# Kernel optimization log

Measured on AMD Instinct MI355X. Metric: run time of the kernel, lower is better.

## Reference

```python
import jax, jax.numpy as jnp
import numpy as np

D = 1024      # feature_dim
H = 16        # heads
HD = D // H   # head_dim
B, N = 8, 1024
LN_EPS = 1e-5


def setup_inputs() -> dict:
    key = jax.random.key(0)
    ks = jax.random.split(key, 12)
    s = 0.02
    return {
        "x": jax.random.normal(ks[0], (B, N, D), jnp.float32),
        "Wq": jax.random.normal(ks[1], (D, D), jnp.float32) * s,
        "bq": jnp.zeros((D,), jnp.float32),
        "Wk": jax.random.normal(ks[2], (D, D), jnp.float32) * s,
        "bk": jnp.zeros((D,), jnp.float32),
        "Wv": jax.random.normal(ks[3], (D, D), jnp.float32) * s,
        "bv": jnp.zeros((D,), jnp.float32),
        "pair_bias": jnp.zeros((D, D), jnp.float32),  # init zeros as in torch
        "Wo": jax.random.normal(ks[4], (D, D), jnp.float32) * s,
        "bo": jnp.zeros((D,), jnp.float32),
        "gamma": jnp.ones((D,), jnp.float32),
        "beta": jnp.zeros((D,), jnp.float32),
    }


def reference(x, Wq, bq, Wk, bk, Wv, bv, pair_bias, Wo, bo, gamma, beta):
    b, n, d = x.shape
    residual = x
    # projections -> [b, h, n, hd]
    def split_heads(t):
        return t.reshape(b, n, H, HD).transpose(0, 2, 1, 3)
    q = split_heads(x @ Wq + bq)
    k = split_heads(x @ Wk + bk)
    v = split_heads(x @ Wv + bv)
    # scores + shared pairwise bias (same bias for every batch/head)
    scores = jnp.einsum('bhqd,bhkd->bhqk', q, k) / jnp.sqrt(jnp.float32(HD))
    scores = scores + pair_bias[:n, :n][None, None, :, :]
    attn = jax.nn.softmax(scores, axis=-1)
    # dropout in eval mode == identity
    out = jnp.einsum('bhqk,bhkd->bhqd', attn, v)
    out = out.transpose(0, 2, 1, 3).reshape(b, n, d)
    out = out @ Wo + bo
    out = residual + out
    # LayerNorm
    mu = jnp.mean(out, axis=-1, keepdims=True)
    var = jnp.var(out, axis=-1, keepdims=True)
    out = (out - mu) * jax.lax.rsqrt(var + LN_EPS) * gamma + beta
    return out, attn
```

## Files before the change

### kernel.cpp

```cpp
#include <hip/hip_runtime.h>
#include <hip/hip_bf16.h>
#include <stdint.h>
#include <stddef.h>

#define DI __device__ __forceinline__

typedef unsigned short u16;
typedef float f32x4 __attribute__((ext_vector_type(4)));
typedef short bf16x8 __attribute__((ext_vector_type(8)));
typedef u16 u16x4 __attribute__((ext_vector_type(4)));

constexpr int Mm = 8192;
constexpr int Dd = 1024;
constexpr float LOG2E = 1.44269504088896f;

DI u16 bf(float f) {
  __hip_bfloat16 h = __float2bfloat16(f);
  return *reinterpret_cast<u16*>(&h);
}

DI float b2f(short s) {
  union { float f; unsigned u; } v;
  v.u = ((unsigned)(unsigned short)s) << 16;
  return v.f;
}

DI f32x4 mfma16(bf16x8 a, bf16x8 b, f32x4 c) {
  return __builtin_amdgcn_mfma_f32_16x16x32_bf16(a, b, c, 0, 0, 0);
}

DI void gload16(const u16* g, u16* l) {
  __builtin_amdgcn_global_load_lds(
      (const __attribute__((address_space(1))) void*)(g),
      (__attribute__((address_space(3))) void*)(l), 16, 0, 0);
}

__global__ __launch_bounds__(256) void k_prep(const float* __restrict__ x,
                                              u16* __restrict__ xb,
                                              const float* __restrict__ pb,
                                              u16* __restrict__ pbb,
                                              const float* __restrict__ W0,
                                              const float* __restrict__ W1,
                                              const float* __restrict__ W2,
                                              const float* __restrict__ W3,
                                              u16* __restrict__ T0,
                                              u16* __restrict__ T1,
                                              u16* __restrict__ T2,
                                              u16* __restrict__ T3) {
  __shared__ float t[32][33];
  const int bid = blockIdx.x;
  const int tid = threadIdx.x;
  if (bid < 8192) {
    size_t i = (size_t)bid * 256 + tid;
    float4 v = *(const float4*)(x + i * 4);
    u16x4 r;
    r.x = bf(v.x); r.y = bf(v.y); r.z = bf(v.z); r.w = bf(v.w);
    *(u16x4*)(xb + i * 4) = r;
  } else if (bid < 9216) {
    size_t i = (size_t)(bid - 8192) * 256 + tid;
    float4 v = *(const float4*)(pb + i * 4);
    u16x4 r;
    r.x = bf(v.x * LOG2E); r.y = bf(v.y * LOG2E);
    r.z = bf(v.z * LOG2E); r.w = bf(v.w * LOG2E);
    *(u16x4*)(pbb + i * 4) = r;
  } else {
    const int tt = bid - 9216;
    const int z = tt >> 10;
    const int rem = tt & 1023;
    const float* W;
    u16* T;
    switch (z) {
      case 0: W = W0; T = T0; break;
      case 1: W = W1; T = T1; break;
      case 2: W = W2; T = T2; break;
      default: W = W3; T = T3; break;
    }
    const int bx = (rem & 31) * 32;
    const int by = (rem >> 5) * 32;
    const int tx = tid & 31, ty = tid >> 5;
#pragma unroll
    for (int i = 0; i < 4; ++i)
      t[ty + i * 8][tx] = W[(size_t)(bx + ty + i * 8) * 1024 + by + tx];
    __syncthreads();
#pragma unroll
    for (int i = 0; i < 4; ++i)
      T[(size_t)(by + ty + i * 8) * 1024 + bx + tx] = bf(t[tx][ty + i * 8]);
  }
}

__global__ __launch_bounds__(256) void k_gemm_qkv(const u16* __restrict__ A,
                                                  const u16* __restrict__ wqT,
                                                  const u16* __restrict__ wkT,
                                                  const u16* __restrict__ wvT,
                                                  const float* __restrict__ bq,
                                                  const float* __restrict__ bk,
                                                  const float* __restrict__ bv,
                                                  u16* __restrict__ qo,
                                                  u16* __restrict__ ko,
                                                  u16* __restrict__ vo) {
  __shared__ __align__(16) u16 smem[2 * 128 * 64];
  u16* As = smem;
  u16* Bs = smem + 128 * 64;
  const int bid = blockIdx.x;
  const int wgid = (bid & 7) * 192 + (bid >> 3);
  const int mode = wgid >> 9;
  const int rem = wgid & 511;
  const int brow = (rem >> 3) * 128;
  const int bcol = (rem & 7) * 128;
  const u16* WT = mode == 0 ? wqT : (mode == 1 ? wkT : wvT);
  const float* bias = mode == 0 ? bq : (mode == 1 ? bk : bv);
  const int tid = threadIdx.x;
  const int lane = tid & 63;
  const int wave = tid >> 6;
  const int wr = (wave >> 1) * 64;
  const int wc = (wave & 1) * 64;
  const int l15 = lane & 15, l4 = lane >> 4;

  f32x4 acc[4][4] = {};
  const int crow0 = tid >> 3;
  const int kpos = (tid & 7) * 8;

  for (int t = 0; t < 16; ++t) {
    const int k0 = t * 64;
#pragma unroll
    for (int r = 0; r < 4; ++r) {
      int crow = r * 32 + crow0;
      u16* ldsbase_a = As + ((r * 256 + wave * 64) << 3);
      u16* ldsbase_b = Bs + ((r * 256 + wave * 64) << 3);
      gload16(A + (size_t)(brow + crow) * 1024 + k0 + kpos, ldsbase_a);
      gload16(WT + (size_t)(bcol + crow) * 1024 + k0 + kpos, ldsbase_b);
    }
    __syncthreads();
#pragma unroll
    for (int kk = 0; kk < 2; ++kk) {
      bf16x8 af[4], bg[4];
      const int kb = kk * 32 + l4 * 8;
#pragma unroll
      for (int mt = 0; mt < 4; ++mt)
        af[mt] = *(const bf16x8*)(As + (wr + mt * 16 + l15) * 64 + kb);
#pragma unroll
      for (int nt = 0; nt < 4; ++nt)
        bg[nt] = *(const bf16x8*)(Bs + (wc + nt * 16 + l15) * 64 + kb);
#pragma unroll
      for (int mt = 0; mt < 4; ++mt)
#pragma unroll
        for (int nt = 0; nt < 4; ++nt)
          acc[mt][nt] = mfma16(af[mt], bg[nt], acc[mt][nt]);
    }
    __syncthreads();
  }

  if (mode == 2) {
#pragma unroll
    for (int nt = 0; nt < 4; ++nt) {
      int dl = wc + nt * 16 + l15;
      float bvv = bias[bcol + dl];
#pragma unroll
      for (int mt = 0; mt < 4; ++mt) {
        int s4 = wr + mt * 16 + l4 * 4;
        u16x4 pk;
        pk.x = bf(acc[mt][nt][0] + bvv);
        pk.y = bf(acc[mt][nt][1] + bvv);
        pk.z = bf(acc[mt][nt][2] + bvv);
        pk.w = bf(acc[mt][nt][3] + bvv);
        *(u16x4*)(smem + dl * 128 + (s4 ^ ((dl & 7) << 3))) = pk;
      }
    }
    __syncthreads();
    const int bb = brow >> 10;
    const int seq0 = brow & 1023;
    const int chunk = tid & 15;
#pragma unroll
    for (int p = 0; p < 8; ++p) {
      int dl = p * 16 + (tid >> 4);
      bf16x8 v = *(const bf16x8*)(smem + dl * 128 + ((chunk * 8) ^ ((dl & 7) << 3)));
      *(bf16x8*)(vo + ((size_t)bb * 1024 + bcol + dl) * 1024 + seq0 + chunk * 8) = v;
    }
    return;
  }

  u16* outp = mode == 0 ? qo : ko;
  const float scale = mode == 0 ? (0.125f * LOG2E) : 1.0f;
#pragma unroll
  for (int nt = 0; nt < 4; ++nt) {
    int gc = bcol + wc + nt * 16 + l15;
    float bvv = bias[gc];
#pragma unroll
    for (int mt = 0; mt < 4; ++mt) {
#pragma unroll
      for (int i = 0; i < 4; ++i) {
        int gm = brow + wr + mt * 16 + l4 * 4 + i;
        outp[(size_t)gm * 1024 + gc] = bf((acc[mt][nt][i] + bvv) * scale);
      }
    }
  }
}

__global__ __launch_bounds__(256) void k_gemm_o(const u16* __restrict__ A,
                                                const u16* __restrict__ WT,
                                                const float* __restrict__ bias,
                                                const float* __restrict__ resid,
                                                float* __restrict__ outp) {
  __shared__ __align__(16) u16 smem[2 * 128 * 64];
  u16* As = smem;
  u16* Bs = smem + 128 * 64;
  const int bid = blockIdx.x;
  const int wgid = (bid & 7) * 64 + (bid >> 3);
  const int brow = (wgid >> 3) * 128;
  const int bcol = (wgid & 7) * 128;
  const int tid = threadIdx.x;
  const int lane = tid & 63;
  const int wave = tid >> 6;
  const int wr = (wave >> 1) * 64;
  const int wc = (wave & 1) * 64;
  const int l15 = lane & 15, l4 = lane >> 4;

  f32x4 acc[4][4] = {};
  const int crow0 = tid >> 3;
  const int kpos = (tid & 7) * 8;

  for (int t = 0; t < 16; ++t) {
    const int k0 = t * 64;
#pragma unroll
    for (int r = 0; r < 4; ++r) {
      int crow = r * 32 + crow0;
      u16* ldsbase_a = As + ((r * 256 + wave * 64) << 3);
      u16* ldsbase_b = Bs + ((r * 256 + wave * 64) << 3);
      gload16(A + (size_t)(brow + crow) * 1024 + k0 + kpos, ldsbase_a);
      gload16(WT + (size_t)(bcol + crow) * 1024 + k0 + kpos, ldsbase_b);
    }
    __syncthreads();
#pragma unroll
    for (int kk = 0; kk < 2; ++kk) {
      bf16x8 af[4], bg[4];
      const int kb = kk * 32 + l4 * 8;
#pragma unroll
      for (int mt = 0; mt < 4; ++mt)
        af[mt] = *(const bf16x8*)(As + (wr + mt * 16 + l15) * 64 + kb);
#pragma unroll
      for (int nt = 0; nt < 4; ++nt)
        bg[nt] = *(const bf16x8*)(Bs + (wc + nt * 16 + l15) * 64 + kb);
#pragma unroll
      for (int mt = 0; mt < 4; ++mt)
#pragma unroll
        for (int nt = 0; nt < 4; ++nt)
          acc[mt][nt] = mfma16(af[mt], bg[nt], acc[mt][nt]);
    }
    __syncthreads();
  }

#pragma unroll
  for (int nt = 0; nt < 4; ++nt) {
    int gc = bcol + wc + nt * 16 + l15;
    float bvv = bias[gc];
#pragma unroll
    for (int mt = 0; mt < 4; ++mt) {
#pragma unroll
      for (int i = 0; i < 4; ++i) {
        int gm = brow + wr + mt * 16 + l4 * 4 + i;
        outp[(size_t)gm * 1024 + gc] =
            acc[mt][nt][i] + bvv + resid[(size_t)gm * 1024 + gc];
      }
    }
  }
}

__global__ __launch_bounds__(256, 3) void k_attn(const u16* __restrict__ q,
                                                 const u16* __restrict__ kk_,
                                                 const u16* __restrict__ vt,
                                                 const u16* __restrict__ pbb,
                                                 float* __restrict__ attn_out,
                                                 u16* __restrict__ aout) {
  __shared__ __align__(16) u16 sc[16 * 1024];
  __shared__ __align__(16) u16 kst[8192];
  __shared__ float invbuf[16];
  const int tid = threadIdx.x;
  const int lane = tid & 63;
  const int wave = tid >> 6;
  const int bid = blockIdx.x;
  const int swz = (bid & 7) * 1024 + (bid >> 3);
  const int bh = swz >> 6;
  const int q0 = (swz & 63) * 16;
  const int b = bh >> 4, h = bh & 15;
  const int l15 = lane & 15, l4 = lane >> 4;
  const int srow8 = (lane >> 3) & 7;
  const int sgsw = (lane & 7) ^ srow8;

  bf16x8 qf0, qf1;
  {
    const u16* qp = q + ((size_t)(b * 1024 + q0 + l15)) * 1024 + h * 64 + l4 * 8;
    qf0 = *(const bf16x8*)qp;
    qf1 = *(const bf16x8*)(qp + 32);
  }

  {
    u16* const kw = kst + wave * 2048;
    const int kvb = wave * 256;
    const u16* kbase = kk_ + (size_t)(b * 1024 + kvb) * 1024 + h * 64 + sgsw * 8;
    gload16(kbase + (size_t)srow8 * 1024, kw);
    gload16(kbase + (size_t)(8 + srow8) * 1024, kw + 512);
    for (int c = 0; c < 16; ++c) {
      if (c < 15) {
        const u16* nsrc = kbase + (size_t)((c + 1) * 16 + srow8) * 1024;
        u16* ndst = kw + ((c + 1) & 1) * 1024;
        gload16(nsrc, ndst);
        gload16(nsrc + 8 * 1024, ndst + 512);
        asm volatile("s_waitcnt vmcnt(2)" ::: "memory");
      } else {
        asm volatile("s_waitcnt vmcnt(0)" ::: "memory");
      }
      __builtin_amdgcn_sched_barrier(0);
      const u16* kb = kw + (c & 1) * 1024;
      const int r = l15;
      bf16x8 k0 = *(const bf16x8*)(kb + r * 64 + ((l4 ^ (r & 7)) << 3));
      bf16x8 k1 = *(const bf16x8*)(kb + r * 64 + (((4 + l4) ^ (r & 7)) << 3));
      f32x4 cc = {};
      cc = mfma16(k0, qf0, cc);
      cc = mfma16(k1, qf1, cc);
      const int c4 = kvb + c * 16 + l4 * 4;
      u16x4 pk;
      pk.x = bf(cc[0]); pk.y = bf(cc[1]); pk.z = bf(cc[2]); pk.w = bf(cc[3]);
      *(u16x4*)(sc + l15 * 1024 + (c4 ^ ((l15 & 7) << 3))) = pk;
    }
  }
  __syncthreads();

  const u16* vbase2 = vt + (size_t)(b * 1024 + h * 64 + wave * 32 + srow8) * 1024 + sgsw * 8;
  u16* const kw3 = kst + wave * 4096;
  if (wave < 2) {
#pragma unroll
    for (int i = 0; i < 4; ++i)
      gload16(vbase2 + (size_t)(i * 8) * 1024, kw3 + i * 512);
  }

  const int r2 = tid >> 4;
  const int l2 = tid & 15;
  {
    const int rx = (r2 & 7) << 3;
    u16* rowp = sc + r2 * 1024;
    const u16* pbrow = pbb + (size_t)(q0 + r2) * 1024 + l2 * 8;
    bf16x8 R[8];
#pragma unroll
    for (int g = 0; g < 8; ++g) {
      bf16x8 v = *(const bf16x8*)(rowp + ((g * 128 + l2 * 8) ^ rx));
      bf16x8 pv = *(const bf16x8*)(pbrow + g * 128);
      bf16x8 s;
#pragma unroll
      for (int j = 0; j < 8; ++j) s[j] = (short)bf(b2f(v[j]) + b2f(pv[j]));
      R[g] = s;
    }
    float mx = -3e38f;
#pragma unroll
    for (int g = 0; g < 8; ++g)
#pragma unroll
      for (int j = 0; j < 8; ++j) mx = fmaxf(mx, b2f(R[g][j]));
#pragma unroll
    for (int o = 1; o < 16; o <<= 1) mx = fmaxf(mx, __shfl_xor(mx, o));
    float sum = 0.f;
#pragma unroll
    for (int g = 0; g < 8; ++g) {
      bf16x8 e;
#pragma unroll
      for (int j = 0; j < 8; ++j) {
        float t = exp2f(b2f(R[g][j]) - mx);
        sum += t;
        e[j] = (short)bf(t);
      }
      *(bf16x8*)(rowp + ((g * 128 + l2 * 8) ^ rx)) = e;
    }
#pragma unroll
    for (int o = 1; o < 16; o <<= 1) sum += __shfl_xor(sum, o);
    if (l2 == 0) invbuf[r2] = 1.f / sum;
  }
  __syncthreads();

  if (wave < 2) {
    f32x4 oacc[2] = {};
    for (int c = 0; c < 16; ++c) {
      if (c < 15) {
        const u16* nsrc = vbase2 + (c + 1) * 64;
        u16* ndst = kw3 + ((c + 1) & 1) * 2048;
#pragma unroll
        for (int i = 0; i < 4; ++i)
          gload16(nsrc + (size_t)(i * 8) * 1024, ndst + i * 512);
        asm volatile("s_waitcnt vmcnt(4)" ::: "memory");
      } else {
        asm volatile("s_waitcnt vmcnt(0)" ::: "memory");
      }
      __builtin_amdgcn_sched_barrier(0);
      const u16* vb = kw3 + (c & 1) * 2048;
#pragma unroll
      for (int ks = 0; ks < 2; ++ks) {
        const int gg = ks * 4 + l4;
        const int e = c * 64 + ks * 32 + l4 * 8;
        bf16x8 pf = *(const bf16x8*)(sc + l15 * 1024 + (e ^ ((l15 & 7) << 3)));
#pragma unroll
        for (int dg = 0; dg < 2; ++dg) {
          const int vr = dg * 16 + l15;
          bf16x8 vf = *(const bf16x8*)(vb + vr * 64 + ((gg ^ (vr & 7)) << 3));
          oacc[dg] = mfma16(pf, vf, oacc[dg]);
        }
      }
    }
#pragma unroll
    for (int dg = 0; dg < 2; ++dg)
#pragma unroll
      for (int i = 0; i < 4; ++i) {
        float iv = invbuf[l4 * 4 + i];
        aout[(size_t)(b * 1024 + q0 + l4 * 4 + i) * 1024 + h * 64 + wave * 32 +
             dg * 16 + l15] = bf(oacc[dg][i] * iv);
      }
  } else {
    const int tid2 = tid - 128;
#pragma unroll
    for (int it = 0; it < 32; ++it) {
      const int row = it >> 1;
      const int col4 = (it & 1) * 128 + tid2;
      const int ebase = (col4 * 4) ^ ((row & 7) << 3);
      u16x4 p = *(const u16x4*)(sc + row * 1024 + ebase);
      const float iv = invbuf[row];
      f32x4 w;
      w[0] = b2f((short)p.x) * iv;
      w[1] = b2f((short)p.y) * iv;
      w[2] = b2f((short)p.z) * iv;
      w[3] = b2f((short)p.w) * iv;
      __builtin_nontemporal_store(
          w, (f32x4*)(attn_out + ((size_t)bh * 1024 + q0 + row) * 1024 + col4 * 4));
    }
  }
}

__global__ __launch_bounds__(256) void k_ln(const float* __restrict__ y,
                                            const float* __restrict__ g,
                                            const float* __restrict__ be,
                                            float* __restrict__ o) {
  const int lane = threadIdx.x & 63;
  const int wave = threadIdx.x >> 6;
  size_t row = (size_t)blockIdx.x * 4 + wave;
  const float* yr = y + row * 1024;
  float4 v[4];
  float s = 0.f, sq = 0.f;
#pragma unroll
  for (int i = 0; i < 4; ++i) {
    v[i] = *(const float4*)(yr + i * 256 + lane * 4);
    s += v[i].x + v[i].y + v[i].z + v[i].w;
    sq += v[i].x * v[i].x + v[i].y * v[i].y + v[i].z * v[i].z + v[i].w * v[i].w;
  }
#pragma unroll
  for (int off = 1; off < 64; off <<= 1) {
    s += __shfl_xor(s, off);
    sq += __shfl_xor(sq, off);
  }
  float mu = s * (1.f / 1024.f);
  float var = sq * (1.f / 1024.f) - mu * mu;
  float rs = rsqrtf(fmaxf(var, 0.f) + 1e-5f);
  float* orow = o + row * 1024;
#pragma unroll
  for (int i = 0; i < 4; ++i) {
    int c = i * 256 + lane * 4;
    float4 gg = *(const float4*)(g + c);
    float4 bb = *(const float4*)(be + c);
    float4 rr;
    rr.x = (v[i].x - mu) * rs * gg.x + bb.x;
    rr.y = (v[i].y - mu) * rs * gg.y + bb.y;
    rr.z = (v[i].z - mu) * rs * gg.z + bb.z;
    rr.w = (v[i].w - mu) * rs * gg.w + bb.w;
    *(float4*)(orow + c) = rr;
  }
}

extern "C" void kernel_launch(void* const* d_in, const int* in_sizes, int n_in,
                              void* d_out, int out_size, void* d_ws, size_t ws_size,
                              hipStream_t stream) {
  const float* x = (const float*)d_in[0];
  const float* Wq = (const float*)d_in[1];
  const float* bq = (const float*)d_in[2];
  const float* Wk = (const float*)d_in[3];
  const float* bk = (const float*)d_in[4];
  const float* Wv = (const float*)d_in[5];
  const float* bv = (const float*)d_in[6];
  const float* pb = (const float*)d_in[7];
  const float* Wo = (const float*)d_in[8];
  const float* bo = (const float*)d_in[9];
  const float* gamma = (const float*)d_in[10];
  const float* beta = (const float*)d_in[11];

  char* ws = (char*)d_ws;
  u16* xb = (u16*)(ws);
  u16* aows = (u16*)(ws);
  u16* wqT = (u16*)(ws + (16u << 20));
  u16* wkT = (u16*)(ws + (18u << 20));
  u16* wvT = (u16*)(ws + (20u << 20));
  u16* woT = (u16*)(ws + (22u << 20));
  u16* qws = (u16*)(ws + (24u << 20));
  u16* kws = (u16*)(ws + (40u << 20));
  u16* vtws = (u16*)(ws + (56u << 20));
  float* yws = (float*)(ws + (72u << 20));
  u16* pbb = (u16*)(ws + (72u << 20));

  float* out_ln = (float*)d_out;
  float* out_attn = out_ln + (size_t)Mm * Dd;

  k_prep<<<13312, 256, 0, stream>>>(x, xb, pb, pbb, Wq, Wk, Wv, Wo,
                                    wqT, wkT, wvT, woT);
  k_gemm_qkv<<<1536, 256, 0, stream>>>(xb, wqT, wkT, wvT,
                                       bq, bk, bv, qws, kws, vtws);
  k_attn<<<8192, 256, 0, stream>>>(qws, kws, vtws, pbb, out_attn, aows);
  k_gemm_o<<<512, 256, 0, stream>>>(aows, woT, bo, x, yws);
  k_ln<<<2048, 256, 0, stream>>>(yws, gamma, beta, out_ln);
}
```

Measured before the change: 305.6 us.

## Double-buffer LDS tiles in QKV and output GEMMs and stage epilogue stores through LDS

Both the QKV projection GEMM and the output projection GEMM now use two LDS buffers. The next K-tile's global-to-LDS loads are issued before the MFMA work on the current tile, so memory latency overlaps with compute, and the loop needs one barrier per iteration instead of two. The epilogues now write results into a swizzled LDS tile and then emit coalesced 16-byte global stores, replacing scattered 2-byte and 4-byte per-element stores; the residual is also read as vectors. LDS use doubles to 64KB per block, which may reduce occupancy.

After: 300.7 us (median of 2 runs). No clear change (-1.6%).

```diff
diff --git a/kernel.cpp b/kernel.cpp
--- a/kernel.cpp
+++ b/kernel.cpp
@@ -98,9 +98,7 @@
                                                   u16* __restrict__ qo,
                                                   u16* __restrict__ ko,
                                                   u16* __restrict__ vo) {
-  __shared__ __align__(16) u16 smem[2 * 128 * 64];
-  u16* As = smem;
-  u16* Bs = smem + 128 * 64;
+  __shared__ __align__(16) u16 smem[2][16384];
   const int bid = blockIdx.x;
   const int wgid = (bid & 7) * 192 + (bid >> 3);
   const int mode = wgid >> 9;
@@ -120,17 +118,33 @@
   const int crow0 = tid >> 3;
   const int kpos = (tid & 7) * 8;
 
+#pragma unroll
+  for (int r = 0; r < 4; ++r) {
+    int crow = r * 32 + crow0;
+    gload16(A + (size_t)(brow + crow) * 1024 + kpos,
+            &smem[0][0] + ((r * 256 + wave * 64) << 3));
+    gload16(WT + (size_t)(bcol + crow) * 1024 + kpos,
+            &smem[0][0] + 8192 + ((r * 256 + wave * 64) << 3));
+  }
+  asm volatile("s_waitcnt vmcnt(0)" ::: "memory");
+  __builtin_amdgcn_s_barrier();
+
   for (int t = 0; t < 16; ++t) {
-    const int k0 = t * 64;
-#pragma unroll
-    for (int r = 0; r < 4; ++r) {
-      int crow = r * 32 + crow0;
-      u16* ldsbase_a = As + ((r * 256 + wave * 64) << 3);
-      u16* ldsbase_b = Bs + ((r * 256 + wave * 64) << 3);
-      gload16(A + (size_t)(brow + crow) * 1024 + k0 + kpos, ldsbase_a);
-      gload16(WT + (size_t)(bcol + crow) * 1024 + k0 + kpos, ldsbase_b);
-    }
-    __syncthreads();
+    const int cur = t & 1;
+    if (t < 15) {
+      const int k0 = (t + 1) * 64;
+#pragma unroll
+      for (int r = 0; r < 4; ++r) {
+        int crow = r * 32 + crow0;
+        gload16(A + (size_t)(brow + crow) * 1024 + k0 + kpos,
+                &smem[cur ^ 1][0] + ((r * 256 + wave * 64) << 3));
+        gload16(WT + (size_t)(bcol + crow) * 1024 + k0 + kpos,
+                &smem[cur ^ 1][0] + 8192 + ((r * 256 + wave * 64) << 3));
+      }
+      __builtin_amdgcn_sched_barrier(0);
+    }
+    const u16* As = &smem[cur][0];
+    const u16* Bs = As + 8192;
 #pragma unroll
     for (int kk = 0; kk < 2; ++kk) {
       bf16x8 af[4], bg[4];
@@ -147,8 +161,16 @@
         for (int nt = 0; nt < 4; ++nt)
           acc[mt][nt] = mfma16(af[mt], bg[nt], acc[mt][nt]);
     }
-    __syncthreads();
-  }
+    if (t < 15) {
+      asm volatile("s_waitcnt vmcnt(0)" ::: "memory");
+      __builtin_amdgcn_sched_barrier(0);
+      __builtin_amdgcn_s_barrier();
+      __builtin_amdgcn_sched_barrier(0);
+    }
+  }
+  __syncthreads();
+
+  u16* tile = &smem[0][0];
 
   if (mode == 2) {
 #pragma unroll
@@ -163,7 +185,7 @@
         pk.y = bf(acc[mt][nt][1] + bvv);
         pk.z = bf(acc[mt][nt][2] + bvv);
         pk.w = bf(acc[mt][nt][3] + bvv);
-        *(u16x4*)(smem + dl * 128 + (s4 ^ ((dl & 7) << 3))) = pk;
+        *(u16x4*)(tile + dl * 128 + (s4 ^ ((dl & 7) << 3))) = pk;
       }
     }
     __syncthreads();
@@ -173,26 +195,34 @@
 #pragma unroll
     for (int p = 0; p < 8; ++p) {
       int dl = p * 16 + (tid >> 4);
-      bf16x8 v = *(const bf16x8*)(smem + dl * 128 + ((chunk * 8) ^ ((dl & 7) << 3)));
+      bf16x8 v = *(const bf16x8*)(tile + dl * 128 + ((chunk * 8) ^ ((dl & 7) << 3)));
       *(bf16x8*)(vo + ((size_t)bb * 1024 + bcol + dl) * 1024 + seq0 + chunk * 8) = v;
     }
     return;
   }
 
+  const float scale = mode == 0 ? (0.125f * LOG2E) : 1.0f;
+#pragma unroll
+  for (int nt = 0; nt < 4; ++nt) {
+    int cl = wc + nt * 16 + l15;
+    float bvv = bias[bcol + cl];
+#pragma unroll
+    for (int mt = 0; mt < 4; ++mt) {
+#pragma unroll
+      for (int i = 0; i < 4; ++i) {
+        int rw = wr + mt * 16 + l4 * 4 + i;
+        tile[rw * 128 + (cl ^ ((rw & 7) << 3))] = bf((acc[mt][nt][i] + bvv) * scale);
+      }
+    }
+  }
+  __syncthreads();
   u16* outp = mode == 0 ? qo : ko;
-  const float scale = mode == 0 ? (0.125f * LOG2E) : 1.0f;
-#pragma unroll
-  for (int nt = 0; nt < 4; ++nt) {
-    int gc = bcol + wc + nt * 16 + l15;
-    float bvv = bias[gc];
-#pragma unroll
-    for (int mt = 0; mt < 4; ++mt) {
-#pragma unroll
-      for (int i = 0; i < 4; ++i) {
-        int gm = brow + wr + mt * 16 + l4 * 4 + i;
-        outp[(size_t)gm * 1024 + gc] = bf((acc[mt][nt][i] + bvv) * scale);
-      }
-    }
+#pragma unroll
+  for (int p = 0; p < 8; ++p) {
+    int rw = p * 16 + (tid >> 4);
+    int c0 = (tid & 15) * 8;
+    bf16x8 v = *(const bf16x8*)(tile + rw * 128 + (c0 ^ ((rw & 7) << 3)));
+    *(bf16x8*)(outp + (size_t)(brow + rw) * 1024 + bcol + c0) = v;
   }
 }
 
@@ -201,9 +231,7 @@
                                                 const float* __restrict__ bias,
                                                 const float* __restrict__ resid,
                                                 float* __restrict__ outp) {
-  __shared__ __align__(16) u16 smem[2 * 128 * 64];
-  u16* As = smem;
-  u16* Bs = smem + 128 * 64;
+  __shared__ __align__(16) u16 smem[2][16384];
   const int bid = blockIdx.x;
   const int wgid = (bid & 7) * 64 + (bid >> 3);
   const int brow = (wgid >> 3) * 128;
@@ -219,17 +247,33 @@
   const int crow0 = tid >> 3;
   const int kpos = (tid & 7) * 8;
 
+#pragma unroll
+  for (int r = 0; r < 4; ++r) {
+    int crow = r * 32 + crow0;
+    gload16(A + (size_t)(brow + crow) * 1024 + kpos,
+            &smem[0][0] + ((r * 256 + wave * 64) << 3));
+    gload16(WT + (size_t)(bcol + crow) * 1024 + kpos,
+            &smem[0][0] + 8192 + ((r * 256 + wave * 64) << 3));
+  }
+  asm volatile("s_waitcnt vmcnt(0)" ::: "memory");
+  __builtin_amdgcn_s_barrier();
+
   for (int t = 0; t < 16; ++t) {
-    const int k0 = t * 64;
-#pragma unroll
-    for (int r = 0; r < 4; ++r) {
-      int crow = r * 32 + crow0;
-      u16* ldsbase_a = As + ((r * 256 + wave * 64) << 3);
-      u16* ldsbase_b = Bs + ((r * 256 + wave * 64) << 3);
-      gload16(A + (size_t)(brow + crow) * 1024 + k0 + kpos, ldsbase_a);
-      gload16(WT + (size_t)(bcol + crow) * 1024 + k0 + kpos, ldsbase_b);
-    }
-    __syncthreads();
+    const int cur = t & 1;
+    if (t < 15) {
+      const int k0 = (t + 1) * 64;
+#pragma unroll
+      for (int r = 0; r < 4; ++r) {
+        int crow = r * 32 + crow0;
+        gload16(A + (size_t)(brow + crow) * 1024 + k0 + kpos,
+                &smem[cur ^ 1][0] + ((r * 256 + wave * 64) << 3));
+        gload16(WT + (size_t)(bcol + crow) * 1024 + k0 + kpos,
+                &smem[cur ^ 1][0] + 8192 + ((r * 256 + wave * 64) << 3));
+      }
+      __builtin_amdgcn_sched_barrier(0);
+    }
+    const u16* As = &smem[cur][0];
+    const u16* Bs = As + 8192;
 #pragma unroll
     for (int kk = 0; kk < 2; ++kk) {
       bf16x8 af[4], bg[4];
@@ -246,22 +290,38 @@
         for (int nt = 0; nt < 4; ++nt)
           acc[mt][nt] = mfma16(af[mt], bg[nt], acc[mt][nt]);
     }
-    __syncthreads();
-  }
-
+    if (t < 15) {
+      asm volatile("s_waitcnt vmcnt(0)" ::: "memory");
+      __builtin_amdgcn_sched_barrier(0);
+      __builtin_amdgcn_s_barrier();
+      __builtin_amdgcn_sched_barrier(0);
+    }
+  }
+  __syncthreads();
+
+  float* ftile = (float*)&smem[0][0];
 #pragma unroll
   for (int nt = 0; nt < 4; ++nt) {
-    int gc = bcol + wc + nt * 16 + l15;
-    float bvv = bias[gc];
-#pragma unroll
-    for (int mt = 0; mt < 4; ++mt) {
+    int cl = wc + nt * 16 + l15;
+    float bvv = bias[bcol + cl];
+#pragma unroll
+    for (int mt = 0; mt < 4; ++mt)
 #pragma unroll
       for (int i = 0; i < 4; ++i) {
-        int gm = brow + wr + mt * 16 + l4 * 4 + i;
-        outp[(size_t)gm * 1024 + gc] =
-            acc[mt][nt][i] + bvv + resid[(size_t)gm * 1024 + gc];
-      }
-    }
+        int rw = wr + mt * 16 + l4 * 4 + i;
+        ftile[rw * 128 + (cl ^ ((rw & 7) << 3))] = acc[mt][nt][i] + bvv;
+      }
+  }
+  __syncthreads();
+#pragma unroll
+  for (int it = 0; it < 16; ++it) {
+    int idx = it * 256 + tid;
+    int rw = idx >> 5;
+    int c4 = idx & 31;
+    f32x4 y = *(const f32x4*)(ftile + rw * 128 + ((c4 * 4) ^ ((rw & 7) << 3)));
+    f32x4 rs = *(const f32x4*)(resid + (size_t)(brow + rw) * 1024 + bcol + c4 * 4);
+    y[0] += rs[0]; y[1] += rs[1]; y[2] += rs[2]; y[3] += rs[3];
+    *(f32x4*)(outp + (size_t)(brow + rw) * 1024 + bcol + c4 * 4) = y;
   }
 }
 
```
